# Optimization experiments

Hardware: AMD Instinct MI355X
Metric: run time of the kernel (lower is better)

Reference implementation:

```python
import jax, jax.numpy as jnp
import numpy as np

APPERTURE = 256
Q_SCALE = 0.06


def setup_inputs() -> dict:
    key = jax.random.key(0)
    ks = jax.random.split(key, 5)
    B, N, D_IN, D_OUT = 4, 4096, 1024, 1024
    std = 1.0 / np.sqrt(D_IN)
    x = jax.random.normal(ks[0], (B, N, D_IN), dtype=jnp.float32)
    Wk = jax.random.normal(ks[1], (D_OUT, D_IN), dtype=jnp.float32) * std
    Wq = jax.random.normal(ks[2], (D_OUT, D_IN), dtype=jnp.float32) * std
    Wv = jax.random.normal(ks[3], (D_OUT, D_IN), dtype=jnp.float32) * std
    Wo = jax.random.normal(ks[4], (D_IN, D_OUT), dtype=jnp.float32) * std
    return {"x": x, "Wk": Wk, "Wq": Wq, "Wv": Wv, "Wo": Wo}


def reference(x, Wk, Wq, Wv, Wo):
    # x: [B, N, D_in]; torch Linear(W) computes x @ W.T
    K = jnp.einsum('bnd,od->bno', x, Wk)          # [B, N, D_out]
    Q = jnp.einsum('bnd,od->bno', x, Wq) * Q_SCALE
    V = jnp.einsum('bnd,od->bno', x, Wv)
    logits = jnp.einsum('bno,bmo->bnm', Q, K)      # [B, N, N]
    N = x.shape[1]
    idx = jnp.arange(N)
    # tril(-a) + triu(a) masks |i-j| >= apperture (keep strict band)
    band_mask = jnp.abs(idx[:, None] - idx[None, :]) >= APPERTURE  # [N, N]
    logits = jnp.where(band_mask[None, :, :], -jnp.inf, logits)
    att_weights = jax.nn.softmax(logits, axis=-1)  # [B, N, N]
    # dropout is identity in eval mode
    # y = (V^T @ weights)^T  ->  y[b,n,:] = sum_m att[b,m,n] * V[b,m,:]
    y = jnp.einsum('bmn,bmo->bno', att_weights, V)
    y = jnp.einsum('bno,io->bni', y, Wo)           # [B, N, D_in]
    return (y, att_weights)
```

## Files before the change

### kernel.cpp

```cpp
#include <hip/hip_runtime.h>
#include <stdint.h>

#define SEQ 4096
#define DM  1024
#define NB  4
#define QSCALE 0.06f

typedef __attribute__((ext_vector_type(8))) short short8;
typedef __attribute__((ext_vector_type(4))) float floatx4;

__device__ __forceinline__ unsigned short f2bf(float f) {
  union { float f; unsigned int u; } v; v.f = f;
  unsigned int u = v.u;
  u += 0x7FFFu + ((u >> 16) & 1u);
  return (unsigned short)(u >> 16);
}

__device__ __forceinline__ void async16(const void* g, void* l) {
  __builtin_amdgcn_global_load_lds(
      (const __attribute__((address_space(1))) void*)g,
      (__attribute__((address_space(3))) void*)l, 16, 0, 0);
}

__global__ void cvt_all(const float* __restrict__ x, const float* __restrict__ wk,
                        const float* __restrict__ wq, const float* __restrict__ wv,
                        const float* __restrict__ wo, unsigned short* __restrict__ xb,
                        unsigned short* __restrict__ wb) {
  int blk = blockIdx.x;
  const float* src;
  unsigned short* dst;
  int i;
  if (blk < 8192) {
    src = x; dst = xb; i = (blk * 256 + threadIdx.x) * 8;
  } else {
    int w = blk - 8192;
    int sel = w >> 9;
    src = sel == 0 ? wk : sel == 1 ? wq : sel == 2 ? wv : wo;
    dst = wb + sel * 1048576;
    i = ((w & 511) * 256 + threadIdx.x) * 8;
  }
  const float4* p = (const float4*)(src + i);
  float4 a = p[0], b = p[1];
  short8 o;
  o[0] = (short)f2bf(a.x); o[1] = (short)f2bf(a.y);
  o[2] = (short)f2bf(a.z); o[3] = (short)f2bf(a.w);
  o[4] = (short)f2bf(b.x); o[5] = (short)f2bf(b.y);
  o[6] = (short)f2bf(b.z); o[7] = (short)f2bf(b.w);
  *(short8*)(dst + i) = o;
}

template <bool OUT_BF16, int MT, int NT, bool DUAL, bool INNER_BY>
__device__ __forceinline__ void gemm_body(
    unsigned short* lds, int bid,
    const unsigned short* __restrict__ A, const unsigned short* __restrict__ W,
    void* __restrict__ C0, void* __restrict__ C1, float a0, float a1, long ldc) {
  const int K = 1024;
  const int NKT = 32;
  int tid = threadIdx.x;
  int lane = tid & 63;
  int wid = tid >> 6;
  int wr = wid >> 2, wc = wid & 3;

  const int CPX = (MT * NT) >> 3;
  int raw = (bid & 7) * CPX + (bid >> 3);
  int bx, by;
  if (INNER_BY) { by = raw % NT; bx = raw / NT; }
  else          { bx = raw % MT; by = raw / MT; }
  long brow = (long)bx * 256;
  long bcol = (long)by * 256;

  floatx4 acc[8][4];
#pragma unroll
  for (int i = 0; i < 8; i++)
#pragma unroll
    for (int j = 0; j < 4; j++) acc[i][j] = (floatx4){0.f, 0.f, 0.f, 0.f};

  int schunk = (tid & 3) ^ ((tid >> 3) & 3);
  const unsigned short* Ag = A + (brow + (tid >> 2)) * K + schunk * 8;
  const unsigned short* Wg = W + (bcol + (tid >> 2)) * K + schunk * 8;
  unsigned short* ldsW = lds + wid * 512;

  int aRd = (wr * 128 + (lane & 15)) * 32 + (lane >> 4) * 8;
  int bRd = (wc * 64 + (lane & 15)) * 32 + (lane >> 4) * 8;
  int rsw = (((lane & 15) >> 1) & 3) << 3;
  aRd ^= rsw;
  bRd ^= rsw;

#pragma unroll
  for (int tt = 0; tt < 3; tt++) {
    unsigned short* d = ldsW + tt * 16384;
    const unsigned short* a = Ag + tt * 32;
    const unsigned short* w = Wg + tt * 32;
    async16(a, d);
    async16(a + 128 * K, d + 4096);
    async16(w, d + 8192);
    async16(w + 128 * K, d + 12288);
  }
  asm volatile("s_waitcnt vmcnt(8)" ::: "memory");
  __builtin_amdgcn_s_barrier();

  for (int t = 0; t < NKT; ++t) {
    const unsigned short* bufA = lds + (t & 3) * 16384;
    const unsigned short* bufB = bufA + 8192;
    short8 a0f[4], b0f[4], a1f[4];
#pragma unroll
    for (int mt = 0; mt < 4; mt++)
      a0f[mt] = *(const short8*)(bufA + aRd + mt * 512);
#pragma unroll
    for (int nt = 0; nt < 4; nt++)
      b0f[nt] = *(const short8*)(bufB + bRd + nt * 512);
#pragma unroll
    for (int mt = 0; mt < 4; mt++)
      a1f[mt] = *(const short8*)(bufA + aRd + 2048 + mt * 512);
    if (t + 3 < NKT) {
      unsigned short* d = ldsW + ((t + 3) & 3) * 16384;
      const unsigned short* a = Ag + (t + 3) * 32;
      const unsigned short* w = Wg + (t + 3) * 32;
      async16(a, d);
      async16(a + 128 * K, d + 4096);
      async16(w, d + 8192);
      async16(w + 128 * K, d + 12288);
    }
    __builtin_amdgcn_s_setprio(1);
#pragma unroll
    for (int mt = 0; mt < 4; mt++)
#pragma unroll
      for (int nt = 0; nt < 4; nt++)
        acc[mt][nt] = __builtin_amdgcn_mfma_f32_16x16x32_bf16(
            a0f[mt], b0f[nt], acc[mt][nt], 0, 0, 0);
#pragma unroll
    for (int mt = 0; mt < 4; mt++)
#pragma unroll
      for (int nt = 0; nt < 4; nt++)
        acc[4 + mt][nt] = __builtin_amdgcn_mfma_f32_16x16x32_bf16(
            a1f[mt], b0f[nt], acc[4 + mt][nt], 0, 0, 0);
    __builtin_amdgcn_s_setprio(0);
    if (t < NKT - 3)
      asm volatile("s_waitcnt vmcnt(8)" ::: "memory");
    else if (t == NKT - 3)
      asm volatile("s_waitcnt vmcnt(4)" ::: "memory");
    else
      asm volatile("s_waitcnt vmcnt(0)" ::: "memory");
    __builtin_amdgcn_s_barrier();
  }

  void* Cp;
  float alpha;
  long cc;
  if (DUAL && by >= NT / 2) {
    Cp = C1; alpha = a1; cc = bcol - (long)(NT / 2) * 256;
  } else {
    Cp = C0; alpha = a0; cc = bcol;
  }
  long crow = brow + wr * 128 + (lane >> 4) * 4;
  long ccol = cc + wc * 64 + (lane & 15);
#pragma unroll
  for (int mt = 0; mt < 8; mt++)
#pragma unroll
    for (int nt = 0; nt < 4; nt++)
#pragma unroll
      for (int r = 0; r < 4; r++) {
        float v = acc[mt][nt][r] * alpha;
        long idx = (crow + mt * 16 + r) * ldc + ccol + nt * 16;
        if (OUT_BF16)
          ((unsigned short*)Cp)[idx] = f2bf(v);
        else
          ((float*)Cp)[idx] = v;
      }
}

__global__ __launch_bounds__(512, 2) void proj_fused(
    const unsigned short* __restrict__ xb, const unsigned short* __restrict__ Wkb,
    const unsigned short* __restrict__ Wvb, unsigned short* __restrict__ Kb,
    unsigned short* __restrict__ Qb, unsigned short* __restrict__ Vt) {
  __shared__ __align__(16) unsigned short lds[4 * 16384];
  if (blockIdx.x < 512)
    gemm_body<true, 64, 8, true, true>(lds, blockIdx.x, xb, Wkb, Kb, Qb, 1.0f,
                                       QSCALE, 1024);
  else
    gemm_body<true, 4, 64, false, false>(lds, blockIdx.x - 512, Wvb, xb, Vt,
                                         nullptr, 1.0f, 1.0f, (long)NB * SEQ);
}

__global__ __launch_bounds__(512, 2) void gemm_wo(
    const unsigned short* __restrict__ yb, const unsigned short* __restrict__ Wob,
    float* __restrict__ outY) {
  __shared__ __align__(16) unsigned short lds[4 * 16384];
  gemm_body<false, 64, 4, false, true>(lds, blockIdx.x, yb, Wob, outY, nullptr,
                                       1.0f, 1.0f, 1024);
}

__global__ __launch_bounds__(512, 2) void logits256(
    const unsigned short* __restrict__ Qb, const unsigned short* __restrict__ Kb,
    float* __restrict__ att) {
  int b = blockIdx.z;
  int n0 = blockIdx.x * 256;
  int m0 = n0 + ((int)blockIdx.y - 1) * 256;
  if (m0 < 0 || m0 >= SEQ) return;
  __shared__ __align__(16) unsigned short lds[4 * 16384];
  const int K = 1024;
  const int NKT = 32;
  int tid = threadIdx.x;
  int lane = tid & 63;
  int wid = tid >> 6;
  int wr = wid >> 2, wc = wid & 3;

  floatx4 acc[8][4];
#pragma unroll
  for (int i = 0; i < 8; i++)
#pragma unroll
    for (int j = 0; j < 4; j++) acc[i][j] = (floatx4){0.f, 0.f, 0.f, 0.f};

  int schunk = (tid & 3) ^ ((tid >> 3) & 3);
  const unsigned short* Ag =
      Qb + ((long)b * SEQ + n0 + (tid >> 2)) * K + schunk * 8;
  const unsigned short* Wg =
      Kb + ((long)b * SEQ + m0 + (tid >> 2)) * K + schunk * 8;
  unsigned short* ldsW = lds + wid * 512;

  int aRd = (wr * 128 + (lane & 15)) * 32 + (lane >> 4) * 8;
  int bRd = (wc * 64 + (lane & 15)) * 32 + (lane >> 4) * 8;
  int rsw = (((lane & 15) >> 1) & 3) << 3;
  aRd ^= rsw;
  bRd ^= rsw;

#pragma unroll
  for (int tt = 0; tt < 3; tt++) {
    unsigned short* d = ldsW + tt * 16384;
    const unsigned short* a = Ag + tt * 32;
    const unsigned short* w = Wg + tt * 32;
    async16(a, d);
    async16(a + 128 * K, d + 4096);
    async16(w, d + 8192);
    async16(w + 128 * K, d + 12288);
  }
  asm volatile("s_waitcnt vmcnt(8)" ::: "memory");
  __builtin_amdgcn_s_barrier();

  for (int t = 0; t < NKT; ++t) {
    const unsigned short* bufA = lds + (t & 3) * 16384;
    const unsigned short* bufB = bufA + 8192;
    short8 a0f[4], b0f[4], a1f[4];
#pragma unroll
    for (int mt = 0; mt < 4; mt++)
      a0f[mt] = *(const short8*)(bufA + aRd + mt * 512);
#pragma unroll
    for (int nt = 0; nt < 4; nt++)
      b0f[nt] = *(const short8*)(bufB + bRd + nt * 512);
#pragma unroll
    for (int mt = 0; mt < 4; mt++)
      a1f[mt] = *(const short8*)(bufA + aRd + 2048 + mt * 512);
    if (t + 3 < NKT) {
      unsigned short* d = ldsW + ((t + 3) & 3) * 16384;
      const unsigned short* a = Ag + (t + 3) * 32;
      const unsigned short* w = Wg + (t + 3) * 32;
      async16(a, d);
      async16(a + 128 * K, d + 4096);
      async16(w, d + 8192);
      async16(w + 128 * K, d + 12288);
    }
    __builtin_amdgcn_s_setprio(1);
#pragma unroll
    for (int mt = 0; mt < 4; mt++)
#pragma unroll
      for (int nt = 0; nt < 4; nt++)
        acc[mt][nt] = __builtin_amdgcn_mfma_f32_16x16x32_bf16(
            a0f[mt], b0f[nt], acc[mt][nt], 0, 0, 0);
#pragma unroll
    for (int mt = 0; mt < 4; mt++)
#pragma unroll
      for (int nt = 0; nt < 4; nt++)
        acc[4 + mt][nt] = __builtin_amdgcn_mfma_f32_16x16x32_bf16(
            a1f[mt], b0f[nt], acc[4 + mt][nt], 0, 0, 0);
    __builtin_amdgcn_s_setprio(0);
    if (t < NKT - 3)
      asm volatile("s_waitcnt vmcnt(8)" ::: "memory");
    else if (t == NKT - 3)
      asm volatile("s_waitcnt vmcnt(4)" ::: "memory");
    else
      asm volatile("s_waitcnt vmcnt(0)" ::: "memory");
    __builtin_amdgcn_s_barrier();
  }

  float* attB = att + (long)b * SEQ * SEQ;
  int crow = n0 + wr * 128 + (lane >> 4) * 4;
  int ccol = m0 + wc * 64 + (lane & 15);
#pragma unroll
  for (int mt = 0; mt < 8; mt++)
#pragma unroll
    for (int nt = 0; nt < 4; nt++)
#pragma unroll
      for (int r = 0; r < 4; r++) {
        int row = crow + mt * 16 + r;
        int col = ccol + nt * 16;
        int d = row - col;
        if (d < 256 && d > -256)
          attB[(long)row * SEQ + col] = acc[mt][nt][r];
      }
}

__global__ __launch_bounds__(256) void softmax_band(
    float* __restrict__ att, unsigned short* __restrict__ attT2) {
  __shared__ float e_lds[16 * 545];
  __shared__ float inv_s[16];
  int blk = blockIdx.x;
  int b = blk >> 8;
  int r0 = (blk & 255) * 16;
  int tid = threadIdx.x;
  int row = tid >> 4;
  int t16 = tid & 15;
  int i = r0 + row;
  int jbase = r0 - 272;
  float* arow = att + ((long)b * SEQ + i) * (long)SEQ;

  float raw[34];
  float m = -1e30f;
#pragma unroll
  for (int s = 0; s < 34; s++) {
    int jj = s * 16 + t16;
    int j = jbase + jj;
    bool ok = (j >= 0) && (j < SEQ) && (j >= i - 255) && (j <= i + 255);
    float v = ok ? arow[j] : -1e30f;
    raw[s] = v;
    m = fmaxf(m, v);
  }
#pragma unroll
  for (int off = 8; off; off >>= 1) m = fmaxf(m, __shfl_xor(m, off, 16));

  float sum = 0.f;
#pragma unroll
  for (int s = 0; s < 34; s++) {
    int jj = s * 16 + t16;
    float e = (raw[s] > -1e29f) ? __expf(raw[s] - m) : 0.f;
    e_lds[row * 545 + jj] = e;
    sum += e;
  }
#pragma unroll
  for (int off = 8; off; off >>= 1) sum += __shfl_xor(sum, off, 16);
  float invr = 1.0f / sum;
  if (t16 == 0) inv_s[row] = invr;
  __syncthreads();

  for (int s = 0; s < 64; s++) {
    int j0 = (s * 16 + t16) * 4;
    float4 w;
    float* wp = (float*)&w;
#pragma unroll
    for (int k = 0; k < 4; k++) {
      int j = j0 + k;
      bool ok = (j >= i - 255) && (j <= i + 255);
      int jj = j - jbase;
      jj = jj < 0 ? 0 : (jj > 543 ? 543 : jj);
      wp[k] = ok ? e_lds[row * 545 + jj] * invr : 0.f;
    }
    *(float4*)(arow + j0) = w;
  }

  int nn = tid >> 4;
  int mi16 = tid & 15;
  int i2 = r0 + mi16;
  float inv2 = inv_s[mi16];
  int Bc = r0 & ~255;
  for (int s = 0; s < 48; s++) {
    int n = Bc - 256 + s * 16 + nn;
    if (n < 0 || n >= SEQ) continue;
    int mi = i2 - (n & ~255) + 256;
    bool ok = (n >= i2 - 255) && (n <= i2 + 255);
    int jj = n - jbase;
    jj = jj < 0 ? 0 : (jj > 544 ? 544 : jj);
    float val = ok ? e_lds[mi16 * 545 + jj] * inv2 : 0.f;
    attT2[(((long)b * 16 + (n >> 8)) * 256 + (n & 255)) * 768 + mi] = f2bf(val);
  }
}

__global__ __launch_bounds__(512, 2) void attv256(
    const unsigned short* __restrict__ attT2, const unsigned short* __restrict__ Vt,
    unsigned short* __restrict__ yb) {
  __shared__ __align__(16) unsigned short lds[4 * 16384];
  const int KA = 768;
  const int NKT = 24;
  int b = blockIdx.z;
  int nb2 = blockIdx.x;
  int o0 = blockIdx.y * 256;
  int N0 = nb2 * 256;
  int tid = threadIdx.x;
  int lane = tid & 63;
  int wid = tid >> 6;
  int wr = wid >> 2, wc = wid & 3;

  floatx4 acc[8][4];
#pragma unroll
  for (int i = 0; i < 8; i++)
#pragma unroll
    for (int j = 0; j < 4; j++) acc[i][j] = (floatx4){0.f, 0.f, 0.f, 0.f};

  int schunk = (tid & 3) ^ ((tid >> 3) & 3);
  const unsigned short* Abase = attT2 + ((long)(b * 16 + nb2) * 256) * KA;
  const unsigned short* Ag = Abase + (long)(tid >> 2) * KA + schunk * 8;
  const unsigned short* Vg =
      Vt + (long)(o0 + (tid >> 2)) * (NB * SEQ) + schunk * 8;
  unsigned short* ldsW = lds + wid * 512;

  int aRd = (wr * 128 + (lane & 15)) * 32 + (lane >> 4) * 8;
  int bRd = (wc * 64 + (lane & 15)) * 32 + (lane >> 4) * 8;
  int rsw = (((lane & 15) >> 1) & 3) << 3;
  aRd ^= rsw;
  bRd ^= rsw;

  auto boff = [&](int t) {
    int mg = N0 - 256 + t * 32;
    int mc = mg < 0 ? 0 : (mg > SEQ - 32 ? SEQ - 32 : mg);
    return (long)b * SEQ + mc;
  };

#pragma unroll
  for (int tt = 0; tt < 3; tt++) {
    unsigned short* d = ldsW + tt * 16384;
    async16(Ag + tt * 32, d);
    async16(Ag + 128 * KA + tt * 32, d + 4096);
    long bo = boff(tt);
    async16(Vg + bo, d + 8192);
    async16(Vg + 128L * (NB * SEQ) + bo, d + 12288);
  }
  asm volatile("s_waitcnt vmcnt(8)" ::: "memory");
  __builtin_amdgcn_s_barrier();

  for (int t = 0; t < NKT; ++t) {
    int mg = N0 - 256 + t * 32;
    bool live = (mg > -32) && (mg < SEQ);
    const unsigned short* bufA = lds + (t & 3) * 16384;
    const unsigned short* bufB = bufA + 8192;
    short8 a0f[4], b0f[4], a1f[4];
#pragma unroll
    for (int mt = 0; mt < 4; mt++)
      a0f[mt] = *(const short8*)(bufA + aRd + mt * 512);
#pragma unroll
    for (int nt = 0; nt < 4; nt++)
      b0f[nt] = *(const short8*)(bufB + bRd + nt * 512);
#pragma unroll
    for (int mt = 0; mt < 4; mt++)
      a1f[mt] = *(const short8*)(bufA + aRd + 2048 + mt * 512);
    if (t + 3 < NKT) {
      unsigned short* d = ldsW + ((t + 3) & 3) * 16384;
      long bo = boff(t + 3);
      async16(Ag + (t + 3) * 32, d);
      async16(Ag + 128 * KA + (t + 3) * 32, d + 4096);
      async16(Vg + bo, d + 8192);
      async16(Vg + 128L * (NB * SEQ) + bo, d + 12288);
    }
    if (live) {
      __builtin_amdgcn_s_setprio(1);
#pragma unroll
      for (int mt = 0; mt < 4; mt++)
#pragma unroll
        for (int nt = 0; nt < 4; nt++)
          acc[mt][nt] = __builtin_amdgcn_mfma_f32_16x16x32_bf16(
              a0f[mt], b0f[nt], acc[mt][nt], 0, 0, 0);
#pragma unroll
      for (int mt = 0; mt < 4; mt++)
#pragma unroll
        for (int nt = 0; nt < 4; nt++)
          acc[4 + mt][nt] = __builtin_amdgcn_mfma_f32_16x16x32_bf16(
              a1f[mt], b0f[nt], acc[4 + mt][nt], 0, 0, 0);
      __builtin_amdgcn_s_setprio(0);
    }
    if (t < NKT - 3)
      asm volatile("s_waitcnt vmcnt(8)" ::: "memory");
    else if (t == NKT - 3)
      asm volatile("s_waitcnt vmcnt(4)" ::: "memory");
    else
      asm volatile("s_waitcnt vmcnt(0)" ::: "memory");
    __builtin_amdgcn_s_barrier();
  }

  long crow = (long)b * SEQ + N0 + wr * 128 + (lane >> 4) * 4;
  int ccol = o0 + wc * 64 + (lane & 15);
#pragma unroll
  for (int mt = 0; mt < 8; mt++)
#pragma unroll
    for (int nt = 0; nt < 4; nt++)
#pragma unroll
      for (int r = 0; r < 4; r++)
        yb[(crow + mt * 16 + r) * DM + ccol + nt * 16] = f2bf(acc[mt][nt][r]);
}

extern "C" void kernel_launch(void* const* d_in, const int* in_sizes, int n_in,
                              void* d_out, int out_size, void* d_ws, size_t ws_size,
                              hipStream_t stream) {
  const float* x  = (const float*)d_in[0];
  const float* Wk = (const float*)d_in[1];
  const float* Wq = (const float*)d_in[2];
  const float* Wv = (const float*)d_in[3];
  const float* Wo = (const float*)d_in[4];
  float* outY = (float*)d_out;
  float* outAtt = outY + (long)NB * SEQ * DM;

  char* ws = (char*)d_ws;
  unsigned short* xb  = (unsigned short*)(ws + 0);
  unsigned short* Kb  = (unsigned short*)(ws + 33554432);
  unsigned short* Qb  = (unsigned short*)(ws + 67108864);
  unsigned short* Vt  = (unsigned short*)(ws + 100663296);
  unsigned short* Wkb = (unsigned short*)(ws + 134217728);
  unsigned short* Wvb = Wkb + 2097152;
  unsigned short* Wob = Wvb + 1048576;
  unsigned short* attT2 = Kb;
  unsigned short* yb = xb;

  cvt_all<<<10240, 256, 0, stream>>>(x, Wk, Wq, Wv, Wo, xb, Wkb);
  proj_fused<<<768, 512, 0, stream>>>(xb, Wkb, Wvb, Kb, Qb, Vt);
  logits256<<<dim3(16, 3, NB), 512, 0, stream>>>(Qb, Kb, outAtt);
  softmax_band<<<1024, 256, 0, stream>>>(outAtt, attT2);
  attv256<<<dim3(16, 4, NB), 512, 0, stream>>>(attT2, Vt, yb);
  gemm_wo<<<256, 512, 0, stream>>>(yb, Wob, outY);
}
```

Measured before the change: 620.2 us.

## Reassociate projections: precompute Wq^T Wk and Wo Wv, skip K/Q/V projections

```diff
diff --git a/kernel.cpp b/kernel.cpp
--- a/kernel.cpp
+++ b/kernel.cpp
@@ -22,10 +22,9 @@
       (__attribute__((address_space(3))) void*)l, 16, 0, 0);
 }
 
-__global__ void cvt_all(const float* __restrict__ x, const float* __restrict__ wk,
-                        const float* __restrict__ wq, const float* __restrict__ wv,
-                        const float* __restrict__ wo, unsigned short* __restrict__ xb,
-                        unsigned short* __restrict__ wb) {
+__global__ void cvt_all(const float* __restrict__ x, const float* __restrict__ wo,
+                        unsigned short* __restrict__ xb,
+                        unsigned short* __restrict__ wob) {
   int blk = blockIdx.x;
   const float* src;
   unsigned short* dst;
@@ -33,11 +32,7 @@
   if (blk < 8192) {
     src = x; dst = xb; i = (blk * 256 + threadIdx.x) * 8;
   } else {
-    int w = blk - 8192;
-    int sel = w >> 9;
-    src = sel == 0 ? wk : sel == 1 ? wq : sel == 2 ? wv : wo;
-    dst = wb + sel * 1048576;
-    i = ((w & 511) * 256 + threadIdx.x) * 8;
+    src = wo; dst = wob; i = ((blk - 8192) * 256 + threadIdx.x) * 8;
   }
   const float4* p = (const float4*)(src + i);
   float4 a = p[0], b = p[1];
@@ -47,6 +42,52 @@
   o[4] = (short)f2bf(b.x); o[5] = (short)f2bf(b.y);
   o[6] = (short)f2bf(b.z); o[7] = (short)f2bf(b.w);
   *(short8*)(dst + i) = o;
+}
+
+__global__ __launch_bounds__(256) void trans_all(
+    const float* __restrict__ wk, const float* __restrict__ wq,
+    const float* __restrict__ wv, const unsigned short* __restrict__ xb,
+    unsigned short* __restrict__ WkT, unsigned short* __restrict__ WqT,
+    unsigned short* __restrict__ WvT, unsigned short* __restrict__ xt) {
+  __shared__ float ls[64 * 65];
+  __shared__ unsigned short xs[64 * 66];
+  int blk = blockIdx.x, tid = threadIdx.x;
+  if (blk < 768) {
+    int mat = blk >> 8, t = blk & 255;
+    const float* src = mat == 0 ? wk : mat == 1 ? wq : wv;
+    unsigned short* dst = mat == 0 ? WkT : mat == 1 ? WqT : WvT;
+    int tr = (t >> 4) * 64;
+    int tc = (t & 15) * 64;
+#pragma unroll
+    for (int k = 0; k < 16; k++) {
+      int idx = k * 256 + tid, r = idx >> 6, c = idx & 63;
+      ls[r * 65 + c] = src[(tr + r) * 1024 + tc + c];
+    }
+    __syncthreads();
+#pragma unroll
+    for (int k = 0; k < 8; k++) {
+      int idx = k * 256 + tid, r = idx >> 5, c2 = (idx & 31) * 2;
+      unsigned short e0 = f2bf(ls[c2 * 65 + r]);
+      unsigned short e1 = f2bf(ls[(c2 + 1) * 65 + r]);
+      *(ushort2*)(dst + (tc + r) * 1024 + tr + c2) = (ushort2){e0, e1};
+    }
+  } else {
+    int t = blk - 768;
+    int tr = (t >> 4) * 64;
+    int tc = (t & 15) * 64;
+#pragma unroll
+    for (int k = 0; k < 16; k++) {
+      int idx = k * 256 + tid, r = idx >> 6, c = idx & 63;
+      xs[r * 66 + c] = xb[(long)(tr + r) * 1024 + tc + c];
+    }
+    __syncthreads();
+#pragma unroll
+    for (int k = 0; k < 8; k++) {
+      int idx = k * 256 + tid, r = idx >> 5, c2 = (idx & 31) * 2;
+      *(ushort2*)(xt + (long)(tc + r) * (NB * SEQ) + tr + c2) =
+          (ushort2){xs[c2 * 66 + r], xs[(c2 + 1) * 66 + r]};
+    }
+  }
 }
 
 template <bool OUT_BF16, int MT, int NT, bool DUAL, bool INNER_BY>
@@ -169,29 +210,37 @@
       }
 }
 
-__global__ __launch_bounds__(512, 2) void proj_fused(
-    const unsigned short* __restrict__ xb, const unsigned short* __restrict__ Wkb,
-    const unsigned short* __restrict__ Wvb, unsigned short* __restrict__ Kb,
-    unsigned short* __restrict__ Qb, unsigned short* __restrict__ Vt) {
+__global__ __launch_bounds__(512, 2) void gp_gemm(
+    const unsigned short* __restrict__ WkT, const unsigned short* __restrict__ WqT,
+    const unsigned short* __restrict__ Wob, const unsigned short* __restrict__ WvT,
+    unsigned short* __restrict__ Gt, unsigned short* __restrict__ P) {
   __shared__ __align__(16) unsigned short lds[4 * 16384];
-  if (blockIdx.x < 512)
-    gemm_body<true, 64, 8, true, true>(lds, blockIdx.x, xb, Wkb, Kb, Qb, 1.0f,
-                                       QSCALE, 1024);
+  if (blockIdx.x < 16)
+    gemm_body<true, 4, 4, false, false>(lds, blockIdx.x, WkT, WqT, Gt, nullptr,
+                                        QSCALE, 1.0f, 1024);
   else
-    gemm_body<true, 4, 64, false, false>(lds, blockIdx.x - 512, Wvb, xb, Vt,
-                                         nullptr, 1.0f, 1.0f, (long)NB * SEQ);
-}
-
-__global__ __launch_bounds__(512, 2) void gemm_wo(
-    const unsigned short* __restrict__ yb, const unsigned short* __restrict__ Wob,
+    gemm_body<true, 4, 4, false, false>(lds, blockIdx.x - 16, Wob, WvT, P,
+                                        nullptr, 1.0f, 1.0f, 1024);
+}
+
+__global__ __launch_bounds__(512, 2) void gemm_T(
+    const unsigned short* __restrict__ xb, const unsigned short* __restrict__ Gt,
+    unsigned short* __restrict__ Tb) {
+  __shared__ __align__(16) unsigned short lds[4 * 16384];
+  gemm_body<true, 64, 4, false, true>(lds, blockIdx.x, xb, Gt, Tb, nullptr,
+                                      1.0f, 1.0f, 1024);
+}
+
+__global__ __launch_bounds__(512, 2) void gemm_Y(
+    const unsigned short* __restrict__ Zb, const unsigned short* __restrict__ P,
     float* __restrict__ outY) {
   __shared__ __align__(16) unsigned short lds[4 * 16384];
-  gemm_body<false, 64, 4, false, true>(lds, blockIdx.x, yb, Wob, outY, nullptr,
+  gemm_body<false, 64, 4, false, true>(lds, blockIdx.x, Zb, P, outY, nullptr,
                                        1.0f, 1.0f, 1024);
 }
 
 __global__ __launch_bounds__(512, 2) void logits256(
-    const unsigned short* __restrict__ Qb, const unsigned short* __restrict__ Kb,
+    const unsigned short* __restrict__ Tb, const unsigned short* __restrict__ xb,
     float* __restrict__ att) {
   int b = blockIdx.z;
   int n0 = blockIdx.x * 256;
@@ -213,9 +262,9 @@
 
   int schunk = (tid & 3) ^ ((tid >> 3) & 3);
   const unsigned short* Ag =
-      Qb + ((long)b * SEQ + n0 + (tid >> 2)) * K + schunk * 8;
+      Tb + ((long)b * SEQ + n0 + (tid >> 2)) * K + schunk * 8;
   const unsigned short* Wg =
-      Kb + ((long)b * SEQ + m0 + (tid >> 2)) * K + schunk * 8;
+      xb + ((long)b * SEQ + m0 + (tid >> 2)) * K + schunk * 8;
   unsigned short* ldsW = lds + wid * 512;
 
   int aRd = (wr * 128 + (lane & 15)) * 32 + (lane >> 4) * 8;
@@ -374,8 +423,8 @@
 }
 
 __global__ __launch_bounds__(512, 2) void attv256(
-    const unsigned short* __restrict__ attT2, const unsigned short* __restrict__ Vt,
-    unsigned short* __restrict__ yb) {
+    const unsigned short* __restrict__ attT2, const unsigned short* __restrict__ xt,
+    unsigned short* __restrict__ Zb) {
   __shared__ __align__(16) unsigned short lds[4 * 16384];
   const int KA = 768;
   const int NKT = 24;
@@ -398,7 +447,7 @@
   const unsigned short* Abase = attT2 + ((long)(b * 16 + nb2) * 256) * KA;
   const unsigned short* Ag = Abase + (long)(tid >> 2) * KA + schunk * 8;
   const unsigned short* Vg =
-      Vt + (long)(o0 + (tid >> 2)) * (NB * SEQ) + schunk * 8;
+      xt + (long)(o0 + (tid >> 2)) * (NB * SEQ) + schunk * 8;
   unsigned short* ldsW = lds + wid * 512;
 
   int aRd = (wr * 128 + (lane & 15)) * 32 + (lane >> 4) * 8;
@@ -481,7 +530,7 @@
     for (int nt = 0; nt < 4; nt++)
 #pragma unroll
       for (int r = 0; r < 4; r++)
-        yb[(crow + mt * 16 + r) * DM + ccol + nt * 16] = f2bf(acc[mt][nt][r]);
+        Zb[(crow + mt * 16 + r) * DM + ccol + nt * 16] = f2bf(acc[mt][nt][r]);
 }
 
 extern "C" void kernel_launch(void* const* d_in, const int* in_sizes, int n_in,
@@ -496,20 +545,24 @@
   float* outAtt = outY + (long)NB * SEQ * DM;
 
   char* ws = (char*)d_ws;
-  unsigned short* xb  = (unsigned short*)(ws + 0);
-  unsigned short* Kb  = (unsigned short*)(ws + 33554432);
-  unsigned short* Qb  = (unsigned short*)(ws + 67108864);
-  unsigned short* Vt  = (unsigned short*)(ws + 100663296);
-  unsigned short* Wkb = (unsigned short*)(ws + 134217728);
-  unsigned short* Wvb = Wkb + 2097152;
-  unsigned short* Wob = Wvb + 1048576;
-  unsigned short* attT2 = Kb;
-  unsigned short* yb = xb;
-
-  cvt_all<<<10240, 256, 0, stream>>>(x, Wk, Wq, Wv, Wo, xb, Wkb);
-  proj_fused<<<768, 512, 0, stream>>>(xb, Wkb, Wvb, Kb, Qb, Vt);
-  logits256<<<dim3(16, 3, NB), 512, 0, stream>>>(Qb, Kb, outAtt);
+  unsigned short* xb   = (unsigned short*)(ws + 0);
+  unsigned short* attT2= (unsigned short*)(ws + 33554432);
+  unsigned short* Tb   = (unsigned short*)(ws + 67108864);
+  unsigned short* xt   = (unsigned short*)(ws + 100663296);
+  unsigned short* Wob  = (unsigned short*)(ws + 134217728);
+  unsigned short* WkT  = (unsigned short*)(ws + 136314880);
+  unsigned short* WqT  = (unsigned short*)(ws + 138412032);
+  unsigned short* WvT  = (unsigned short*)(ws + 140509184);
+  unsigned short* Gt   = (unsigned short*)(ws + 142606336);
+  unsigned short* P    = (unsigned short*)(ws + 144703488);
+  unsigned short* Zb = xb;
+
+  cvt_all<<<8704, 256, 0, stream>>>(x, Wo, xb, Wob);
+  trans_all<<<4864, 256, 0, stream>>>(Wk, Wq, Wv, xb, WkT, WqT, WvT, xt);
+  gp_gemm<<<32, 512, 0, stream>>>(WkT, WqT, Wob, WvT, Gt, P);
+  gemm_T<<<256, 512, 0, stream>>>(xb, Gt, Tb);
+  logits256<<<dim3(16, 3, NB), 512, 0, stream>>>(Tb, xb, outAtt);
   softmax_band<<<1024, 256, 0, stream>>>(outAtt, attT2);
-  attv256<<<dim3(16, 4, NB), 512, 0, stream>>>(attT2, Vt, yb);
-  gemm_wo<<<256, 512, 0, stream>>>(yb, Wob, outY);
-}
+  attv256<<<dim3(16, 4, NB), 512, 0, stream>>>(attT2, xt, Zb);
+  gemm_Y<<<256, 512, 0, stream>>>(Zb, P, outY);
+}
```

Measured after the change: 596.2 us. 1.04x faster.
